# Optimization experiments

Hardware: AMD Instinct MI355X
Metric: run time of the kernel (lower is better)

## Reference

```python
import jax, jax.numpy as jnp
import numpy as np

B, L, C_IN, HID = 32, 2048, 256, 512


def setup_inputs() -> dict:
    key = jax.random.key(0)
    k1, k2, k3, k4, k5, k6 = jax.random.split(key, 6)
    x = jax.random.normal(k1, (B, L, C_IN), dtype=jnp.float32)
    y = jax.random.normal(k2, (B, L, C_IN), dtype=jnp.float32)
    # Conv1d kernel_size=1 weights, stored as [out, in] (squeezed kernel dim)
    s1 = 1.0 / np.sqrt(C_IN)
    s2 = 1.0 / np.sqrt(HID)
    W1 = jax.random.uniform(k3, (HID, C_IN), jnp.float32, -s1, s1)
    b1 = jax.random.uniform(k4, (HID,), jnp.float32, -s1, s1)
    W2 = jax.random.uniform(k5, (HID, HID), jnp.float32, -s2, s2)
    b2 = jax.random.uniform(k6, (HID,), jnp.float32, -s2, s2)
    return {"x": x, "y": y, "W1": W1, "b1": b1, "W2": W2, "b2": b2}


def _project(t, W1, b1, W2, b2):
    # t: [B, L, C_in] -> (transpose + two 1x1 convs) -> [B, HID, L]
    h = jnp.einsum('hc,blc->bhl', W1, t) + b1[None, :, None]
    h = jnp.einsum('gh,bhl->bgl', W2, h) + b2[None, :, None]
    return h


def reference(x, y, W1, b1, W2, b2):
    xp = _project(x, W1, b1, W2, b2)  # [B, HID, L]
    yp = _project(y, W1, b1, W2, b2)  # [B, HID, L]
    # grouped conv1d with groups=B*M and full-length kernel == per-channel dot product
    out = jnp.sum(jnp.tanh(xp) * jnp.tanh(yp), axis=-1)  # [B, HID]
    return out
```

## Files before the change

### kernel.cpp

```cpp
#include <hip/hip_runtime.h>
#include <hip/hip_bf16.h>

#define B_   32
#define L_   2048
#define CIN  256
#define HID  512
#define TL   16
#define TPT  16
#define NGRP 256
#define NBLK (NGRP * 4)

#define TANH_SCALE 2.885390081777927

typedef __bf16 bf16_t;
typedef __bf16 bf16x8 __attribute__((ext_vector_type(8)));
typedef __bf16 bf16x4 __attribute__((ext_vector_type(4)));
typedef float  f32x4  __attribute__((ext_vector_type(4)));

#define APIPE  8192u
#define ABUF   16384u
#define TY_OFF 32768u

__global__ void compose_kernel(const float* __restrict__ W1, const float* __restrict__ W2,
                               const float* __restrict__ b1, const float* __restrict__ b2,
                               bf16_t* __restrict__ Wc, float* __restrict__ bc)
{
    const int g = blockIdx.x;
    const int c = threadIdx.x;
    const float* w2row = W2 + (size_t)g * HID;
    float s[8] = {0.f, 0.f, 0.f, 0.f, 0.f, 0.f, 0.f, 0.f};
    for (int h = 0; h < HID; h += 8) {
#pragma unroll
        for (int k = 0; k < 8; ++k)
            s[k] = fmaf(w2row[h + k], W1[(size_t)(h + k) * CIN + c], s[k]);
    }
    float tot = ((s[0] + s[1]) + (s[2] + s[3])) + ((s[4] + s[5]) + (s[6] + s[7]));
    Wc[(size_t)g * CIN + c] = (bf16_t)(tot * (float)TANH_SCALE);
    if (c == 0) {
        float t0 = 0.f, t1 = 0.f;
        for (int h = 0; h < HID; h += 2) {
            t0 = fmaf(w2row[h], b1[h], t0);
            t1 = fmaf(w2row[h + 1], b1[h + 1], t1);
        }
        bc[g] = (t0 + t1 + b2[g]) * (float)TANH_SCALE;
    }
}

__global__ __launch_bounds__(512, 4)
void fused_kernel(const float* __restrict__ x, const float* __restrict__ y,
                  const bf16_t* __restrict__ Wc, const float* __restrict__ bc,
                  float* __restrict__ partial)
{
    __shared__ char U[49152];

    const int tid  = threadIdx.x;
    const int lane = tid & 63;
    const int wv   = tid >> 6;
    const int l15  = lane & 15;
    const int l4   = lane >> 4;

    const int d    = blockIdx.x;
    const int grp  = (d & 7) + 8 * (d >> 5);
    const int q    = (d >> 3) & 3;

    const int pipe = wv >> 2;
    const int wq   = wv & 3;
    const int gc0  = q * 128 + wq * 32;

    bf16x8 wreg[8][2];
#pragma unroll
    for (int kk = 0; kk < 8; ++kk)
#pragma unroll
        for (int cj = 0; cj < 2; ++cj)
            wreg[kk][cj] = *reinterpret_cast<const bf16x8*>(
                Wc + (size_t)(gc0 + cj * 16 + l15) * CIN + kk * 32 + l4 * 8);

    f32x4 bcv[2];
#pragma unroll
    for (int cj = 0; cj < 2; ++cj) {
        float4 t4 = *reinterpret_cast<const float4*>(bc + gc0 + cj * 16 + l4 * 4);
        bcv[cj] = (f32x4){t4.x, t4.y, t4.z, t4.w};
    }

    const int sp = tid >> 8;
    const int t8 = tid & 255;
    const int sr = t8 >> 4;
    const int sq = t8 & 15;
    const unsigned sswz = (unsigned)((sr & 15) << 4);
    const unsigned soff = (unsigned)(sp * APIPE + sr * 512);
    const float* sptr = (sp ? y : x) + ((size_t)grp * (TPT * TL) + sr) * CIN;

    float4 v[4];
    auto sload = [&](const float* rowbase) {
        const float4* s4 = reinterpret_cast<const float4*>(rowbase);
#pragma unroll
        for (int c = 0; c < 4; ++c) v[c] = s4[sq + 16 * c];
    };
    auto swrite = [&](int buf) {
        char* p = U + (unsigned)(buf * ABUF) + soff;
#pragma unroll
        for (int c = 0; c < 4; ++c) {
            const int f = sq + 16 * c;
            bf16x4 h;
            h[0] = (bf16_t)v[c].x; h[1] = (bf16_t)v[c].y;
            h[2] = (bf16_t)v[c].z; h[3] = (bf16_t)v[c].w;
            *reinterpret_cast<bf16x4*>(p + (((unsigned)(8 * f)) ^ sswz)) = h;
        }
    };

    const unsigned abase = (pipe ? APIPE : 0u) +
        (unsigned)(l15 * 512) + (((unsigned)(l4 * 16)) ^ ((unsigned)(l15 << 4)));
    const unsigned tyb = TY_OFF + (unsigned)(wq * 1536 + l15 * 48 + l4 * 8);

    f32x4 psum[2];
    psum[0] = (f32x4){0.f, 0.f, 0.f, 0.f};
    psum[1] = (f32x4){0.f, 0.f, 0.f, 0.f};

    sload(sptr);
    swrite(0);
    __syncthreads();

    for (int t = 0; t < TPT; ++t) {
        const bool pf = (t + 1 < TPT);
        const int cur = t & 1;
        if (pf) {
            sptr += TL * CIN;
            sload(sptr);
        }

        f32x4 acc0 = bcv[0], acc1 = bcv[1];
        const unsigned ab = abase + (unsigned)(cur * ABUF);
        __builtin_amdgcn_s_setprio(1);
#pragma unroll
        for (int kk = 0; kk < 8; ++kk) {
            bf16x8 a = *reinterpret_cast<const bf16x8*>(U + (ab ^ (unsigned)(kk << 6)));
            acc0 = __builtin_amdgcn_mfma_f32_16x16x32_bf16(wreg[kk][0], a, acc0, 0, 0, 0);
            acc1 = __builtin_amdgcn_mfma_f32_16x16x32_bf16(wreg[kk][1], a, acc1, 0, 0, 0);
        }
        __builtin_amdgcn_s_setprio(0);

#pragma unroll
        for (int r2 = 0; r2 < 4; ++r2) {
            acc0[r2] = fmaf(-2.0f, __builtin_amdgcn_rcpf(exp2f(acc0[r2]) + 1.0f), 1.0f);
            acc1[r2] = fmaf(-2.0f, __builtin_amdgcn_rcpf(exp2f(acc1[r2]) + 1.0f), 1.0f);
        }

        if (pipe) {
            bf16x4 t0, t1;
#pragma unroll
            for (int r2 = 0; r2 < 4; ++r2) { t0[r2] = (bf16_t)acc0[r2]; t1[r2] = (bf16_t)acc1[r2]; }
            *reinterpret_cast<bf16x4*>(U + tyb + (unsigned)(cur * 8192))        = t0;
            *reinterpret_cast<bf16x4*>(U + tyb + (unsigned)(cur * 8192) + 768u) = t1;
        }

        if (pf) swrite(cur ^ 1);

        __syncthreads();

        if (!pipe) {
            bf16x4 o0 = *reinterpret_cast<const bf16x4*>(U + tyb + (unsigned)(cur * 8192));
            bf16x4 o1 = *reinterpret_cast<const bf16x4*>(U + tyb + (unsigned)(cur * 8192) + 768u);
#pragma unroll
            for (int r2 = 0; r2 < 4; ++r2) {
                psum[0][r2] = fmaf(acc0[r2], (float)o0[r2], psum[0][r2]);
                psum[1][r2] = fmaf(acc1[r2], (float)o1[r2], psum[1][r2]);
            }
        }
    }

    if (!pipe) {
#pragma unroll
        for (int cj = 0; cj < 2; ++cj)
#pragma unroll
            for (int r2 = 0; r2 < 4; ++r2) {
                float s = psum[cj][r2];
                s += __shfl_xor(s, 1);
                s += __shfl_xor(s, 2);
                s += __shfl_xor(s, 4);
                s += __shfl_xor(s, 8);
                psum[cj][r2] = s;
            }
        if (l15 == 0) {
#pragma unroll
            for (int cj = 0; cj < 2; ++cj) {
                float4 o4 = make_float4(psum[cj][0], psum[cj][1], psum[cj][2], psum[cj][3]);
                *reinterpret_cast<float4*>(partial + (size_t)grp * HID + gc0 + cj * 16 + l4 * 4) = o4;
            }
        }
    }
}

__global__ void reduce_kernel(const float* __restrict__ partial, float* __restrict__ out)
{
    int b = blockIdx.x;
    int g = threadIdx.x;
    float s = 0.f;
#pragma unroll
    for (int k = 0; k < 8; ++k)
        s += partial[((size_t)(b * 8 + k)) * HID + g];
    out[b * HID + g] = s;
}

extern "C" void kernel_launch(void* const* d_in, const int* in_sizes, int n_in,
                              void* d_out, int out_size, void* d_ws, size_t ws_size,
                              hipStream_t stream)
{
    const float* x  = (const float*)d_in[0];
    const float* y  = (const float*)d_in[1];
    const float* W1 = (const float*)d_in[2];
    const float* b1 = (const float*)d_in[3];
    const float* W2 = (const float*)d_in[4];
    const float* b2 = (const float*)d_in[5];
    float* out = (float*)d_out;

    char* ws = (char*)d_ws;
    bf16_t* Wc     = (bf16_t*)ws;
    float*  bc     = (float*)(ws + (256 << 10));
    float*  partial = (float*)(ws + (264 << 10));

    hipLaunchKernelGGL(compose_kernel, dim3(HID), dim3(CIN), 0, stream, W1, W2, b1, b2, Wc, bc);
    hipLaunchKernelGGL(fused_kernel, dim3(NBLK), dim3(512), 0, stream, x, y, Wc, bc, partial);
    hipLaunchKernelGGL(reduce_kernel, dim3(B_), dim3(512), 0, stream, partial, out);
}
```

Baseline: 89.54 us.

## Compute x and y projections in the same wave and drop LDS tanh exchange

Each wave now runs the MFMA projections for both x and y over 32-row tiles, so tanh(x)*tanh(y) is accumulated in registers. This removes the LDS round trip of bf16 tanh values between the two wave pipes. The grid is halved, with each block covering 256 output channels instead of 128. Weights are no longer held in registers; they are reloaded from global/L2 inside the k-loop, and the next tile's global loads are split into two phases to overlap with compute. The trade-off is higher register pressure from 8 accumulators, repeated weight fetches, fewer blocks, and 64KB of LDS per block, which may lower occupancy.

```diff
diff --git a/kernel.cpp b/kernel.cpp
--- a/kernel.cpp
+++ b/kernel.cpp
@@ -5,10 +5,10 @@
 #define L_   2048
 #define CIN  256
 #define HID  512
-#define TL   16
-#define TPT  16
+#define TL   32
+#define TPT  8
 #define NGRP 256
-#define NBLK (NGRP * 4)
+#define NBLK (NGRP * 2)
 
 #define TANH_SCALE 2.885390081777927
 
@@ -17,9 +17,8 @@
 typedef __bf16 bf16x4 __attribute__((ext_vector_type(4)));
 typedef float  f32x4  __attribute__((ext_vector_type(4)));
 
-#define APIPE  8192u
-#define ABUF   16384u
-#define TY_OFF 32768u
+#define APIPE 16384u
+#define ABUF  32768u
 
 __global__ void compose_kernel(const float* __restrict__ W1, const float* __restrict__ W2,
                                const float* __restrict__ b1, const float* __restrict__ b2,
@@ -51,7 +50,7 @@
                   const bf16_t* __restrict__ Wc, const float* __restrict__ bc,
                   float* __restrict__ partial)
 {
-    __shared__ char U[49152];
+    __shared__ char U[65536];
 
     const int tid  = threadIdx.x;
     const int lane = tid & 63;
@@ -60,20 +59,9 @@
     const int l4   = lane >> 4;
 
     const int d    = blockIdx.x;
-    const int grp  = (d & 7) + 8 * (d >> 5);
-    const int q    = (d >> 3) & 3;
-
-    const int pipe = wv >> 2;
-    const int wq   = wv & 3;
-    const int gc0  = q * 128 + wq * 32;
-
-    bf16x8 wreg[8][2];
-#pragma unroll
-    for (int kk = 0; kk < 8; ++kk)
-#pragma unroll
-        for (int cj = 0; cj < 2; ++cj)
-            wreg[kk][cj] = *reinterpret_cast<const bf16x8*>(
-                Wc + (size_t)(gc0 + cj * 16 + l15) * CIN + kk * 32 + l4 * 8);
+    const int grp  = (d & 7) + 8 * (d >> 4);
+    const int half = (d >> 3) & 1;
+    const int gc0  = half * 256 + wv * 32;
 
     f32x4 bcv[2];
 #pragma unroll
@@ -82,110 +70,137 @@
         bcv[cj] = (f32x4){t4.x, t4.y, t4.z, t4.w};
     }
 
-    const int sp = tid >> 8;
-    const int t8 = tid & 255;
-    const int sr = t8 >> 4;
-    const int sq = t8 & 15;
-    const unsigned sswz = (unsigned)((sr & 15) << 4);
-    const unsigned soff = (unsigned)(sp * APIPE + sr * 512);
-    const float* sptr = (sp ? y : x) + ((size_t)grp * (TPT * TL) + sr) * CIN;
-
-    float4 v[4];
-    auto sload = [&](const float* rowbase) {
+    const int sp   = tid >> 8;
+    const int t8   = tid & 255;
+    const int srow = t8 >> 3;
+    const int sq   = t8 & 7;
+    const unsigned sswz = (unsigned)((srow & 15) << 4);
+    const unsigned soff = (unsigned)(sp * APIPE + srow * 512);
+    const float* sptr = (sp ? y : x) + ((size_t)grp * (TPT * TL) + srow) * CIN;
+
+    float4 ve[4], vl[4];
+    auto sloadE = [&](const float* rowbase) {
         const float4* s4 = reinterpret_cast<const float4*>(rowbase);
 #pragma unroll
-        for (int c = 0; c < 4; ++c) v[c] = s4[sq + 16 * c];
-    };
-    auto swrite = [&](int buf) {
+        for (int c = 0; c < 4; ++c) ve[c] = s4[sq + 8 * c];
+    };
+    auto sloadL = [&](const float* rowbase) {
+        const float4* s4 = reinterpret_cast<const float4*>(rowbase);
+#pragma unroll
+        for (int c = 0; c < 4; ++c) vl[c] = s4[sq + 8 * (c + 4)];
+    };
+    auto swriteE = [&](int buf) {
         char* p = U + (unsigned)(buf * ABUF) + soff;
 #pragma unroll
         for (int c = 0; c < 4; ++c) {
-            const int f = sq + 16 * c;
+            const int f = sq + 8 * c;
             bf16x4 h;
-            h[0] = (bf16_t)v[c].x; h[1] = (bf16_t)v[c].y;
-            h[2] = (bf16_t)v[c].z; h[3] = (bf16_t)v[c].w;
+            h[0] = (bf16_t)ve[c].x; h[1] = (bf16_t)ve[c].y;
+            h[2] = (bf16_t)ve[c].z; h[3] = (bf16_t)ve[c].w;
             *reinterpret_cast<bf16x4*>(p + (((unsigned)(8 * f)) ^ sswz)) = h;
         }
     };
-
-    const unsigned abase = (pipe ? APIPE : 0u) +
-        (unsigned)(l15 * 512) + (((unsigned)(l4 * 16)) ^ ((unsigned)(l15 << 4)));
-    const unsigned tyb = TY_OFF + (unsigned)(wq * 1536 + l15 * 48 + l4 * 8);
+    auto swriteL = [&](int buf) {
+        char* p = U + (unsigned)(buf * ABUF) + soff;
+#pragma unroll
+        for (int c = 0; c < 4; ++c) {
+            const int f = sq + 8 * (c + 4);
+            bf16x4 h;
+            h[0] = (bf16_t)vl[c].x; h[1] = (bf16_t)vl[c].y;
+            h[2] = (bf16_t)vl[c].z; h[3] = (bf16_t)vl[c].w;
+            *reinterpret_cast<bf16x4*>(p + (((unsigned)(8 * f)) ^ sswz)) = h;
+        }
+    };
+
+    unsigned ab[2][2];
+#pragma unroll
+    for (int pp = 0; pp < 2; ++pp)
+#pragma unroll
+        for (int ri = 0; ri < 2; ++ri)
+            ab[pp][ri] = (unsigned)(pp * APIPE) + (unsigned)((ri * 16 + l15) * 512) +
+                         (((unsigned)(l4 * 16)) ^ ((unsigned)(l15 << 4)));
 
     f32x4 psum[2];
     psum[0] = (f32x4){0.f, 0.f, 0.f, 0.f};
     psum[1] = (f32x4){0.f, 0.f, 0.f, 0.f};
 
-    sload(sptr);
-    swrite(0);
+    sloadE(sptr); sloadL(sptr);
+    swriteE(0);   swriteL(0);
     __syncthreads();
 
     for (int t = 0; t < TPT; ++t) {
         const bool pf = (t + 1 < TPT);
         const int cur = t & 1;
+        const float* nptr = sptr + TL * CIN;
+        if (pf) sloadE(nptr);
+
+        f32x4 accx[2][2], accy[2][2];
+#pragma unroll
+        for (int ri = 0; ri < 2; ++ri)
+#pragma unroll
+            for (int cj = 0; cj < 2; ++cj) { accx[ri][cj] = bcv[cj]; accy[ri][cj] = bcv[cj]; }
+
+        const unsigned cb = (unsigned)(cur * ABUF);
+        __builtin_amdgcn_s_setprio(1);
+#pragma unroll
+        for (int kk = 0; kk < 8; ++kk) {
+            bf16x8 w[2];
+#pragma unroll
+            for (int cj = 0; cj < 2; ++cj)
+                w[cj] = *reinterpret_cast<const bf16x8*>(
+                    Wc + (size_t)(gc0 + cj * 16 + l15) * CIN + kk * 32 + l4 * 8);
+            const unsigned kx = (unsigned)(kk << 6);
+            bf16x8 ax0 = *reinterpret_cast<const bf16x8*>(U + cb + (ab[0][0] ^ kx));
+            bf16x8 ax1 = *reinterpret_cast<const bf16x8*>(U + cb + (ab[0][1] ^ kx));
+            bf16x8 ay0 = *reinterpret_cast<const bf16x8*>(U + cb + (ab[1][0] ^ kx));
+            bf16x8 ay1 = *reinterpret_cast<const bf16x8*>(U + cb + (ab[1][1] ^ kx));
+#pragma unroll
+            for (int cj = 0; cj < 2; ++cj) {
+                accx[0][cj] = __builtin_amdgcn_mfma_f32_16x16x32_bf16(w[cj], ax0, accx[0][cj], 0, 0, 0);
+                accx[1][cj] = __builtin_amdgcn_mfma_f32_16x16x32_bf16(w[cj], ax1, accx[1][cj], 0, 0, 0);
+                accy[0][cj] = __builtin_amdgcn_mfma_f32_16x16x32_bf16(w[cj], ay0, accy[0][cj], 0, 0, 0);
+                accy[1][cj] = __builtin_amdgcn_mfma_f32_16x16x32_bf16(w[cj], ay1, accy[1][cj], 0, 0, 0);
+            }
+        }
+        __builtin_amdgcn_s_setprio(0);
+
         if (pf) {
-            sptr += TL * CIN;
-            sload(sptr);
-        }
-
-        f32x4 acc0 = bcv[0], acc1 = bcv[1];
-        const unsigned ab = abase + (unsigned)(cur * ABUF);
-        __builtin_amdgcn_s_setprio(1);
-#pragma unroll
-        for (int kk = 0; kk < 8; ++kk) {
-            bf16x8 a = *reinterpret_cast<const bf16x8*>(U + (ab ^ (unsigned)(kk << 6)));
-            acc0 = __builtin_amdgcn_mfma_f32_16x16x32_bf16(wreg[kk][0], a, acc0, 0, 0, 0);
-            acc1 = __builtin_amdgcn_mfma_f32_16x16x32_bf16(wreg[kk][1], a, acc1, 0, 0, 0);
-        }
-        __builtin_amdgcn_s_setprio(0);
-
+            swriteE(cur ^ 1);
+            sloadL(nptr);
+        }
+
+#pragma unroll
+        for (int ri = 0; ri < 2; ++ri)
+#pragma unroll
+            for (int cj = 0; cj < 2; ++cj)
+#pragma unroll
+                for (int r2 = 0; r2 < 4; ++r2) {
+                    float tx = fmaf(-2.0f, __builtin_amdgcn_rcpf(exp2f(accx[ri][cj][r2]) + 1.0f), 1.0f);
+                    float ty = fmaf(-2.0f, __builtin_amdgcn_rcpf(exp2f(accy[ri][cj][r2]) + 1.0f), 1.0f);
+                    psum[cj][r2] = fmaf(tx, ty, psum[cj][r2]);
+                }
+
+        if (pf) swriteL(cur ^ 1);
+        __syncthreads();
+        sptr = nptr;
+    }
+
+#pragma unroll
+    for (int cj = 0; cj < 2; ++cj)
 #pragma unroll
         for (int r2 = 0; r2 < 4; ++r2) {
-            acc0[r2] = fmaf(-2.0f, __builtin_amdgcn_rcpf(exp2f(acc0[r2]) + 1.0f), 1.0f);
-            acc1[r2] = fmaf(-2.0f, __builtin_amdgcn_rcpf(exp2f(acc1[r2]) + 1.0f), 1.0f);
-        }
-
-        if (pipe) {
-            bf16x4 t0, t1;
-#pragma unroll
-            for (int r2 = 0; r2 < 4; ++r2) { t0[r2] = (bf16_t)acc0[r2]; t1[r2] = (bf16_t)acc1[r2]; }
-            *reinterpret_cast<bf16x4*>(U + tyb + (unsigned)(cur * 8192))        = t0;
-            *reinterpret_cast<bf16x4*>(U + tyb + (unsigned)(cur * 8192) + 768u) = t1;
-        }
-
-        if (pf) swrite(cur ^ 1);
-
-        __syncthreads();
-
-        if (!pipe) {
-            bf16x4 o0 = *reinterpret_cast<const bf16x4*>(U + tyb + (unsigned)(cur * 8192));
-            bf16x4 o1 = *reinterpret_cast<const bf16x4*>(U + tyb + (unsigned)(cur * 8192) + 768u);
-#pragma unroll
-            for (int r2 = 0; r2 < 4; ++r2) {
-                psum[0][r2] = fmaf(acc0[r2], (float)o0[r2], psum[0][r2]);
-                psum[1][r2] = fmaf(acc1[r2], (float)o1[r2], psum[1][r2]);
-            }
-        }
-    }
-
-    if (!pipe) {
-#pragma unroll
-        for (int cj = 0; cj < 2; ++cj)
-#pragma unroll
-            for (int r2 = 0; r2 < 4; ++r2) {
-                float s = psum[cj][r2];
-                s += __shfl_xor(s, 1);
-                s += __shfl_xor(s, 2);
-                s += __shfl_xor(s, 4);
-                s += __shfl_xor(s, 8);
-                psum[cj][r2] = s;
-            }
-        if (l15 == 0) {
-#pragma unroll
-            for (int cj = 0; cj < 2; ++cj) {
-                float4 o4 = make_float4(psum[cj][0], psum[cj][1], psum[cj][2], psum[cj][3]);
-                *reinterpret_cast<float4*>(partial + (size_t)grp * HID + gc0 + cj * 16 + l4 * 4) = o4;
-            }
+            float s = psum[cj][r2];
+            s += __shfl_xor(s, 1);
+            s += __shfl_xor(s, 2);
+            s += __shfl_xor(s, 4);
+            s += __shfl_xor(s, 8);
+            psum[cj][r2] = s;
+        }
+    if (l15 == 0) {
+#pragma unroll
+        for (int cj = 0; cj < 2; ++cj) {
+            float4 o4 = make_float4(psum[cj][0], psum[cj][1], psum[cj][2], psum[cj][3]);
+            *reinterpret_cast<float4*>(partial + (size_t)grp * HID + gc0 + cj * 16 + l4 * 4) = o4;
         }
     }
 }
```

Measured after the change: 123.7 us. 38.1% more time.
